# Performance work log

Measured on AMD Instinct MI355X. Metric: run time of the kernel, lower is better.

The kernel has to match this reference:

```python
import jax, jax.numpy as jnp
import numpy as np

N_HEADS = 28
N_KV_HEADS = 4
HEAD_DIM = 128
ROPE_THETA = 1000000.0


def _sinusoidal_positions(num_pos, dim, theta):
    # Mirrors create_sinusoidal_positions: interleaved [sin, cos] pairs -> (num_pos, dim)
    positions = jnp.arange(0, num_pos, dtype=jnp.float32)
    half_dim = dim // 2
    freq_indices = jnp.arange(0, half_dim, dtype=jnp.float32)
    inv_freq = 1.0 / theta ** (freq_indices / half_dim)
    sinusoid_inp = jnp.einsum('i,j->ij', positions, inv_freq)
    return jnp.stack([jnp.sin(sinusoid_inp), jnp.cos(sinusoid_inp)], axis=-1).reshape(num_pos, -1)


def _rotate_half(x):
    x1, x2 = jnp.split(x, 2, axis=-1)
    return jnp.concatenate([-x2, x1], axis=-1)


def _apply_rope(q, k, sinu_pos):
    # Mirrors apply_rotary_pos_emb: split halves, duplicate, rotate_half mixing.
    sin, cos = jnp.split(sinu_pos, 2, axis=-1)
    sin = jnp.concatenate([sin, sin], axis=-1)[None, None, :, :]
    cos = jnp.concatenate([cos, cos], axis=-1)[None, None, :, :]
    q_embed = q * cos + _rotate_half(q) * sin
    k_embed = k * cos + _rotate_half(k) * sin
    return q_embed, k_embed


def setup_inputs() -> dict:
    key = jax.random.key(0)
    ks = jax.random.split(key, 5)
    B, S, H = 2, 2048, 3584
    std = 0.02
    return {
        'hidden_states': jax.random.normal(ks[0], (B, S, H), dtype=jnp.float32),
        'wq': jax.random.normal(ks[1], (H, N_HEADS * HEAD_DIM), dtype=jnp.float32) * std,
        'wk': jax.random.normal(ks[2], (H, N_KV_HEADS * HEAD_DIM), dtype=jnp.float32) * std,
        'wv': jax.random.normal(ks[3], (H, N_KV_HEADS * HEAD_DIM), dtype=jnp.float32) * std,
        'wo': jax.random.normal(ks[4], (N_HEADS * HEAD_DIM, H), dtype=jnp.float32) * std,
    }


def reference(hidden_states, wq, wk, wv, wo):
    B, S, H = hidden_states.shape
    gqa_ratio = N_HEADS // N_KV_HEADS

    # QKV projections (bias-free) and head split -> (B, heads, S, d)
    q = (hidden_states @ wq).reshape(B, S, N_HEADS, HEAD_DIM).transpose(0, 2, 1, 3)
    k = (hidden_states @ wk).reshape(B, S, N_KV_HEADS, HEAD_DIM).transpose(0, 2, 1, 3)
    v = (hidden_states @ wv).reshape(B, S, N_KV_HEADS, HEAD_DIM).transpose(0, 2, 1, 3)

    # Inline RoPE on Q/K
    sincos = _sinusoidal_positions(S, HEAD_DIM, ROPE_THETA)
    q, k = _apply_rope(q, k, sincos)

    # GQA head expansion via tile (matches jnp.tile in source: block-repeat)
    k = jnp.tile(k, (1, gqa_ratio, 1, 1))
    v = jnp.tile(v, (1, gqa_ratio, 1, 1))

    # Causal scaled dot-product attention
    scale = 1.0 / jnp.sqrt(jnp.float32(HEAD_DIM))
    scores = jnp.einsum('bhqd,bhkd->bhqk', q, k) * scale  # (B, H, S, S)
    causal = jnp.tril(jnp.ones((S, S), dtype=bool))
    scores = jnp.where(causal[None, None], scores, jnp.finfo(scores.dtype).min)
    probs = jax.nn.softmax(scores, axis=-1)
    out = jnp.einsum('bhqk,bhkd->bhqd', probs, v)

    # Merge heads and output projection
    out = out.transpose(0, 2, 1, 3).reshape(B, S, N_HEADS * HEAD_DIM)
    return out @ wo
```

## Files before the change

kernel.cpp:

```cpp
#include <hip/hip_runtime.h>
#include <hip/hip_bf16.h>

typedef __attribute__((ext_vector_type(4))) float f32x4;
typedef __attribute__((ext_vector_type(8))) short s16x8;
typedef __attribute__((ext_vector_type(4))) short s16x4;
typedef unsigned short u16;

__device__ __forceinline__ u16 f2bf(float f) {
  union { float f; unsigned int u; } v; v.f = f;
  unsigned int r = v.u + 0x7fffu + ((v.u >> 16) & 1u);
  return (u16)(r >> 16);
}

__device__ __forceinline__ void gload_lds16(const void* g, void* l) {
  __builtin_amdgcn_global_load_lds(
      (const __attribute__((address_space(1))) void*)g,
      (__attribute__((address_space(3))) void*)l, 16, 0, 0);
}

__global__ __launch_bounds__(256) void cvt_bf16(const float* __restrict__ in,
                                                u16* __restrict__ outp, int nquad) {
  int i = blockIdx.x * 256 + threadIdx.x;
  if (i >= nquad) return;
  f32x4 v = *(const f32x4*)(in + (size_t)i * 4);
  s16x4 o;
  o.x = (short)f2bf(v.x); o.y = (short)f2bf(v.y);
  o.z = (short)f2bf(v.z); o.w = (short)f2bf(v.w);
  *(s16x4*)(outp + (size_t)i * 4) = o;
}

__global__ __launch_bounds__(256) void transpose_cvt(const float* __restrict__ in,
                                                     u16* __restrict__ outp, int R, int C) {
  __shared__ float t[32][33];
  int c0 = blockIdx.x * 32, r0 = blockIdx.y * 32;
  int tx = threadIdx.x & 31, ty = threadIdx.x >> 5;
#pragma unroll
  for (int i = 0; i < 32; i += 8) t[ty + i][tx] = in[(size_t)(r0 + ty + i) * C + c0 + tx];
  __syncthreads();
#pragma unroll
  for (int i = 0; i < 32; i += 8)
    outp[(size_t)(c0 + ty + i) * R + r0 + tx] = f2bf(t[tx][ty + i]);
}

__global__ void rope_table(float2* __restrict__ tab) {
  int p = blockIdx.x, e = threadIdx.x;
  int j = e >> 1;
  float f1 = powf(1.0e6f, -(float)j / 64.0f);
  float f2 = powf(1.0e6f, -(float)(j + 32) / 64.0f);
  float a1 = (float)p * f1, a2 = (float)p * f2;
  float S = (e & 1) ? cosf(a1) : sinf(a1);
  float C = (e & 1) ? cosf(a2) : sinf(a2);
  tab[p * 64 + e] = make_float2(S, C);
}

__global__ __launch_bounds__(256) void rope_pack(const float* __restrict__ P,
                                                 const float2* __restrict__ tab,
                                                 u16* __restrict__ outp, int nh, int ldp,
                                                 float scale) {
  int idx = blockIdx.x * 4 + (threadIdx.x >> 6);
  int e = threadIdx.x & 63;
  int s = idx & 2047;
  int bh = idx >> 11;
  int b = bh / nh, h = bh - b * nh;
  size_t prow = ((size_t)(b * 2048 + s)) * (size_t)ldp + (size_t)h * 128;
  float x1 = P[prow + e], x2 = P[prow + e + 64];
  float2 t = tab[s * 64 + e];
  float o1 = (x1 * t.y - x2 * t.x) * scale;
  float o2 = (x2 * t.y + x1 * t.x) * scale;
  size_t orow = (size_t)idx * 128;
  outp[orow + e] = f2bf(o1);
  outp[orow + e + 64] = f2bf(o2);
}

__global__ __launch_bounds__(256) void pack_vt(const float* __restrict__ Vp,
                                               u16* __restrict__ Vt, int ldp, int coff) {
  __shared__ float t[32][33];
  int bk = blockIdx.z;
  int b = bk >> 2, kh = bk & 3;
  int s0 = blockIdx.x * 32, d0 = blockIdx.y * 32;
  int tx = threadIdx.x & 31, ty = threadIdx.x >> 5;
  const float* in = Vp + (size_t)(b * 2048) * ldp + coff + kh * 128;
#pragma unroll
  for (int i = 0; i < 32; i += 8) t[ty + i][tx] = in[(size_t)(s0 + ty + i) * ldp + d0 + tx];
  __syncthreads();
  u16* outp = Vt + (size_t)bk * 128 * 2048;
#pragma unroll
  for (int i = 0; i < 32; i += 8)
    outp[(size_t)(d0 + ty + i) * 2048 + s0 + tx] = f2bf(t[tx][ty + i]);
}

__global__ __launch_bounds__(256) void gemm_bt(const u16* __restrict__ A,
                                               const u16* __restrict__ BT,
                                               float* __restrict__ C, int M, int N, int K) {
  __shared__ u16 lA[128 * 32];
  __shared__ u16 lB[128 * 32];
  const int tid = threadIdx.x;
  const int lane = tid & 63, wave = tid >> 6;
  const int bm = blockIdx.y * 128, bn = blockIdx.x * 128;
  const int wr = (wave >> 1) * 64, wc = (wave & 1) * 64;
  const int r = lane & 15, g = lane >> 4;

  f32x4 acc[4][4];
#pragma unroll
  for (int i = 0; i < 4; i++)
#pragma unroll
    for (int j = 0; j < 4; j++) acc[i][j] = (f32x4){0.f, 0.f, 0.f, 0.f};

  const int o0 = wave * 2048 + lane * 16;
  const int row0 = o0 >> 6, cb0 = (o0 & 63) >> 1;
  const int o1 = o0 + 1024;
  const int row1 = o1 >> 6, cb1 = (o1 & 63) >> 1;
  const u16* a0 = A + (size_t)(bm + row0) * K + cb0;
  const u16* a1 = A + (size_t)(bm + row1) * K + cb1;
  const u16* b0 = BT + (size_t)(bn + row0) * K + cb0;
  const u16* b1 = BT + (size_t)(bn + row1) * K + cb1;
  u16* lA0 = lA + wave * 2 * 512; u16* lA1 = lA + (wave * 2 + 1) * 512;
  u16* lB0 = lB + wave * 2 * 512; u16* lB1 = lB + (wave * 2 + 1) * 512;

  for (int kt = 0; kt < K; kt += 32) {
    __syncthreads();
    gload_lds16(a0 + kt, lA0);
    gload_lds16(a1 + kt, lA1);
    gload_lds16(b0 + kt, lB0);
    gload_lds16(b1 + kt, lB1);
    __syncthreads();
    s16x8 af[4], bf[4];
#pragma unroll
    for (int m2 = 0; m2 < 4; m2++) af[m2] = *(const s16x8*)(lA + (wr + m2 * 16 + r) * 32 + g * 8);
#pragma unroll
    for (int n2 = 0; n2 < 4; n2++) bf[n2] = *(const s16x8*)(lB + (wc + n2 * 16 + r) * 32 + g * 8);
#pragma unroll
    for (int m2 = 0; m2 < 4; m2++)
#pragma unroll
      for (int n2 = 0; n2 < 4; n2++)
        acc[m2][n2] = __builtin_amdgcn_mfma_f32_16x16x32_bf16(af[m2], bf[n2], acc[m2][n2], 0, 0, 0);
  }
#pragma unroll
  for (int m2 = 0; m2 < 4; m2++)
#pragma unroll
    for (int n2 = 0; n2 < 4; n2++)
#pragma unroll
      for (int jj = 0; jj < 4; jj++)
        C[(size_t)(bm + wr + m2 * 16 + g * 4 + jj) * N + (bn + wc + n2 * 16 + r)] =
            acc[m2][n2][jj];
}

__global__ __launch_bounds__(512, 2) void gemm256(const u16* __restrict__ A,
                                                  const u16* __restrict__ BT,
                                                  float* __restrict__ C,
                                                  int M, int N, int K) {
  extern __shared__ u16 sm[];
  const int tid = threadIdx.x;
  const int lane = tid & 63, w = tid >> 6;
  const int wm = w >> 2, wn = w & 3;
  const int r = lane & 15, g = lane >> 4;
  const int bm = blockIdx.y * 256, bn = blockIdx.x * 256;

  f32x4 acc[8][4];
#pragma unroll
  for (int mf = 0; mf < 8; mf++)
#pragma unroll
    for (int nf = 0; nf < 4; nf++) acc[mf][nf] = (f32x4){0.f, 0.f, 0.f, 0.f};

  const int row_s = tid >> 3;
  const int col_s = ((((tid & 7) << 4) ^ ((row_s & 7) << 4)) >> 1);
  const u16* sAg[4]; const u16* sBg[4];
#pragma unroll
  for (int i = 0; i < 4; i++) {
    sAg[i] = A  + (size_t)(bm + i * 64 + row_s) * K + col_s;
    sBg[i] = BT + (size_t)(bn + i * 64 + row_s) * K + col_s;
  }

#pragma unroll
  for (int i = 0; i < 4; i++) gload_lds16(sAg[i], sm + i * 4096 + w * 512);
#pragma unroll
  for (int i = 0; i < 4; i++) gload_lds16(sBg[i], sm + 32768 + i * 4096 + w * 512);

  const int NT = K >> 6;
  const int swz = (r & 7) << 4;
#pragma unroll 1
  for (int t = 0; t < NT; ++t) {
    const int p = t & 1;
    const u16* LA = sm + p * 16384;
    const u16* LB = sm + 32768 + p * 16384;
    u16* SA = sm + (p ^ 1) * 16384;
    u16* SB = sm + 32768 + (p ^ 1) * 16384;
    const int ktn = (t + 1 < NT) ? (t + 1) * 64 : 0;

    __builtin_amdgcn_s_barrier();
    gload_lds16(sAg[0] + ktn, SA + 0 * 4096 + w * 512);
    gload_lds16(sAg[1] + ktn, SA + 1 * 4096 + w * 512);
    asm volatile("s_waitcnt vmcnt(2)" ::: "memory");
    __builtin_amdgcn_s_barrier();
    __builtin_amdgcn_sched_barrier(0);

    const char* Ac = (const char*)LA;
    const char* Bc = (const char*)LB;
    s16x8 bf[4][2];
#pragma unroll
    for (int nf = 0; nf < 4; nf++)
#pragma unroll
      for (int ks = 0; ks < 2; ks++) {
        int row = wn * 64 + nf * 16 + r;
        bf[nf][ks] = *(const s16x8*)(Bc + ((row * 128 + ks * 64 + g * 16) ^ swz));
      }
#pragma unroll
    for (int ph = 0; ph < 4; ph++) {
      if (ph == 1) {
        gload_lds16(sAg[2] + ktn, SA + 2 * 4096 + w * 512);
        gload_lds16(sAg[3] + ktn, SA + 3 * 4096 + w * 512);
      } else if (ph == 2) {
        gload_lds16(sBg[0] + ktn, SB + 0 * 4096 + w * 512);
        gload_lds16(sBg[1] + ktn, SB + 1 * 4096 + w * 512);
      } else if (ph == 3) {
        gload_lds16(sBg[2] + ktn, SB + 2 * 4096 + w * 512);
        gload_lds16(sBg[3] + ktn, SB + 3 * 4096 + w * 512);
      }
      s16x8 af[2][2];
#pragma unroll
      for (int mi = 0; mi < 2; mi++)
#pragma unroll
        for (int ks = 0; ks < 2; ks++) {
          int row = wm * 128 + (ph * 2 + mi) * 16 + r;
          af[mi][ks] = *(const s16x8*)(Ac + ((row * 128 + ks * 64 + g * 16) ^ swz));
        }
      __builtin_amdgcn_s_setprio(1);
#pragma unroll
      for (int mi = 0; mi < 2; mi++)
#pragma unroll
        for (int nf = 0; nf < 4; nf++) {
          acc[ph * 2 + mi][nf] = __builtin_amdgcn_mfma_f32_16x16x32_bf16(
              af[mi][0], bf[nf][0], acc[ph * 2 + mi][nf], 0, 0, 0);
          acc[ph * 2 + mi][nf] = __builtin_amdgcn_mfma_f32_16x16x32_bf16(
              af[mi][1], bf[nf][1], acc[ph * 2 + mi][nf], 0, 0, 0);
        }
      __builtin_amdgcn_s_setprio(0);
    }
  }
  asm volatile("s_waitcnt vmcnt(0)" ::: "memory");

#pragma unroll
  for (int mf = 0; mf < 8; mf++)
#pragma unroll
    for (int nf = 0; nf < 4; nf++)
#pragma unroll
      for (int jj = 0; jj < 4; jj++)
        C[(size_t)(bm + wm * 128 + mf * 16 + g * 4 + jj) * N +
          (bn + wn * 64 + nf * 16 + r)] = acc[mf][nf][jj];
}

__global__ __launch_bounds__(512, 4) void attn_kernel(const u16* __restrict__ Q,
                                                      const u16* __restrict__ K,
                                                      const u16* __restrict__ Vt,
                                                      u16* __restrict__ AO) {
  constexpr int S = 2048, NH = 28, NKV = 4, D = 128;
  __shared__ u16 Kl[2][32 * 128];
  __shared__ u16 Vl[2][32 * 128];
  const int tid = threadIdx.x;
  const int lane = tid & 63, w = tid >> 6;
  const int r = lane & 15, g = lane >> 4;
  const int pp = blockIdx.x, h = blockIdx.y, b = blockIdx.z;
  const int kh = h & 3;
  const u16* Kb = K + ((size_t)(b * NKV + kh) * S) * D;
  const u16* Vb = Vt + ((size_t)(b * NKV + kh) * D) * S;

  const int o = tid * 16;
  const int krow = o >> 8;
  const int kcol = ((o & 255) ^ ((krow & 7) << 4)) >> 1;
  const u16* sK = Kb + (size_t)krow * D + kcol;
  const int pb = o ^ (((o >> 7) & 7) << 4);
  const u16* sV = Vb + (size_t)(pb >> 6) * S + ((pb & 63) >> 1);

#pragma unroll 1
  for (int seg = 0; seg < 2; ++seg) {
    const int qt = seg ? (15 - pp) : pp;
    const int q0 = qt * 128 + w * 16;
    const u16* Qb = Q + ((size_t)(b * NH + h) * S + q0) * D;

    s16x8 qf[4];
#pragma unroll
    for (int kb = 0; kb < 4; kb++)
      qf[kb] = *(const s16x8*)(Qb + (size_t)r * D + kb * 32 + g * 8);

    f32x4 o8[8];
#pragma unroll
    for (int c = 0; c < 8; c++) o8[c] = (f32x4){0.f, 0.f, 0.f, 0.f};
    float m = -1e30f, lsum = 0.f;
    const int qg = q0 + r;
    const int NT = 4 * qt + 4;

    gload_lds16(sK, (u16*)Kl[0] + tid * 8);
    gload_lds16(sV, (u16*)Vl[0] + tid * 8);

    int cur = 0;
#pragma unroll 1
    for (int t = 0; t < NT; ++t) {
      const int j = t * 32;
      if (t + 1 < NT) {
        const int jn = j + 32;
        gload_lds16(sK + (size_t)jn * D, (u16*)Kl[cur ^ 1] + tid * 8);
        gload_lds16(sV + jn, (u16*)Vl[cur ^ 1] + tid * 8);
        asm volatile("s_waitcnt vmcnt(2)" ::: "memory");
      } else {
        asm volatile("s_waitcnt vmcnt(0)" ::: "memory");
      }
      __builtin_amdgcn_s_barrier();
      __builtin_amdgcn_sched_barrier(0);
      if (j <= q0 + 15) {
        f32x4 st0 = (f32x4){0.f, 0.f, 0.f, 0.f};
        f32x4 st1 = (f32x4){0.f, 0.f, 0.f, 0.f};
        const int swz = (r & 7) << 4;
        const char* Kc = (const char*)Kl[cur];
        __builtin_amdgcn_s_setprio(1);
#pragma unroll
        for (int kb = 0; kb < 4; kb++) {
          int cb = (kb * 64 + g * 16) ^ swz;
          s16x8 kf = *(const s16x8*)(Kc + r * 256 + cb);
          st0 = __builtin_amdgcn_mfma_f32_16x16x32_bf16(kf, qf[kb], st0, 0, 0, 0);
        }
#pragma unroll
        for (int kb = 0; kb < 4; kb++) {
          int cb = (kb * 64 + g * 16) ^ swz;
          s16x8 kf = *(const s16x8*)(Kc + (r + 16) * 256 + cb);
          st1 = __builtin_amdgcn_mfma_f32_16x16x32_bf16(kf, qf[kb], st1, 0, 0, 0);
        }
        __builtin_amdgcn_s_setprio(0);
        float s8v[8];
        if (j + 31 <= q0) {
#pragma unroll
          for (int jj = 0; jj < 4; jj++) { s8v[jj] = st0[jj]; s8v[jj + 4] = st1[jj]; }
        } else {
#pragma unroll
          for (int jj = 0; jj < 4; jj++) {
            int kv0 = j + g * 4 + jj;
            s8v[jj] = (kv0 > qg) ? -1e30f : st0[jj];
            s8v[jj + 4] = (kv0 + 16 > qg) ? -1e30f : st1[jj];
          }
        }
        float pm = fmaxf(fmaxf(fmaxf(s8v[0], s8v[1]), fmaxf(s8v[2], s8v[3])),
                         fmaxf(fmaxf(s8v[4], s8v[5]), fmaxf(s8v[6], s8v[7])));
        pm = fmaxf(pm, __shfl_xor(pm, 16));
        pm = fmaxf(pm, __shfl_xor(pm, 32));
        const bool defer = __all(pm <= m + 8.f);
        float mnew, fr;
        if (defer) { mnew = m; fr = 1.f; }
        else { mnew = fmaxf(m, pm); fr = __expf(m - mnew); }
        float pv[8], psum = 0.f;
#pragma unroll
        for (int i2 = 0; i2 < 8; i2++) { pv[i2] = __expf(s8v[i2] - mnew); psum += pv[i2]; }
        psum += __shfl_xor(psum, 16);
        psum += __shfl_xor(psum, 32);
        lsum = lsum * fr + psum;
        m = mnew;
        unsigned pk[4];
#pragma unroll
        for (int i2 = 0; i2 < 4; i2++) {
          __hip_bfloat162 hv = __float22bfloat162_rn(make_float2(pv[2 * i2], pv[2 * i2 + 1]));
          union { __hip_bfloat162 h; unsigned u; } cv; cv.h = hv; pk[i2] = cv.u;
        }
        int L0 = r + ((g & 1) << 5);
        unsigned a0 = (unsigned)__shfl((int)pk[0], L0);
        unsigned a1 = (unsigned)__shfl((int)pk[1], L0);
        unsigned a2 = (unsigned)__shfl((int)pk[2], L0);
        unsigned a3 = (unsigned)__shfl((int)pk[3], L0);
        unsigned b0 = (unsigned)__shfl((int)pk[0], L0 + 16);
        unsigned b1 = (unsigned)__shfl((int)pk[1], L0 + 16);
        unsigned b2 = (unsigned)__shfl((int)pk[2], L0 + 16);
        unsigned b3 = (unsigned)__shfl((int)pk[3], L0 + 16);
        union { unsigned u[4]; s16x8 v; } pu;
        pu.u[0] = (g < 2) ? a0 : a2;
        pu.u[1] = (g < 2) ? a1 : a3;
        pu.u[2] = (g < 2) ? b0 : b2;
        pu.u[3] = (g < 2) ? b1 : b3;
        s16x8 pa = pu.v;
        float fB[4];
        if (!defer) {
#pragma unroll
          for (int jj = 0; jj < 4; jj++) fB[jj] = __shfl(fr, g * 4 + jj);
        }
        const char* Vc = (const char*)Vl[cur];
        __builtin_amdgcn_s_setprio(1);
#pragma unroll
        for (int c = 0; c < 8; c++) {
          int pbyte = (c * 16 + r) * 64 + g * 16;
          int vaddr = pbyte ^ ((r >> 1) << 4);
          s16x8 vf = *(const s16x8*)(Vc + vaddr);
          f32x4 oc = o8[c];
          if (!defer) { oc.x *= fB[0]; oc.y *= fB[1]; oc.z *= fB[2]; oc.w *= fB[3]; }
          o8[c] = __builtin_amdgcn_mfma_f32_16x16x32_bf16(pa, vf, oc, 0, 0, 0);
        }
        __builtin_amdgcn_s_setprio(0);
      }
      __builtin_amdgcn_s_barrier();
      cur ^= 1;
    }

    float lB[4];
#pragma unroll
    for (int jj = 0; jj < 4; jj++) lB[jj] = __shfl(lsum, g * 4 + jj);
#pragma unroll
    for (int c = 0; c < 8; c++)
#pragma unroll
      for (int jj = 0; jj < 4; jj++) {
        float val = o8[c][jj] / lB[jj];
        AO[(size_t)(b * S + q0 + g * 4 + jj) * 3584 + h * 128 + c * 16 + r] = f2bf(val);
      }
  }
}

static const size_t OFF_XBF = 0;
static const size_t OFF_WQT = 29360128;
static const size_t OFF_WKT = 55050240;
static const size_t OFF_WVT = 58720256;
static const size_t OFF_WOT = 62390272;
static const size_t OFF_TAB = 88080384;
static const size_t OFF_QBF = 89128960;
static const size_t OFF_KBF = 118489088;
static const size_t OFF_VT  = 122683392;
static const size_t OFF_QP  = 126877696;
static const size_t OFF_KVP = 185597952;

extern "C" void kernel_launch(void* const* d_in, const int* in_sizes, int n_in,
                              void* d_out, int out_size, void* d_ws, size_t ws_size,
                              hipStream_t stream) {
  const float* X  = (const float*)d_in[0];
  const float* Wq = (const float*)d_in[1];
  const float* Wk = (const float*)d_in[2];
  const float* Wv = (const float*)d_in[3];
  const float* Wo = (const float*)d_in[4];
  float* out = (float*)d_out;
  char* ws = (char*)d_ws;

  u16* Xbf = (u16*)(ws + OFF_XBF);
  u16* WqT = (u16*)(ws + OFF_WQT);
  u16* WkT = (u16*)(ws + OFF_WKT);
  u16* WvT = (u16*)(ws + OFF_WVT);
  u16* WoT = (u16*)(ws + OFF_WOT);
  float2* tab = (float2*)(ws + OFF_TAB);
  u16* Qbf = (u16*)(ws + OFF_QBF);
  u16* Kbf = (u16*)(ws + OFF_KBF);
  u16* Vtb = (u16*)(ws + OFF_VT);
  float* Qp = (float*)(ws + OFF_QP);
  float* KVp = (float*)(ws + OFF_KVP);
  u16* AO  = (u16*)(ws + OFF_QP);

  hipFuncSetAttribute((const void*)gemm256,
                      hipFuncAttributeMaxDynamicSharedMemorySize, 131072);

  cvt_bf16<<<14336, 256, 0, stream>>>(X, Xbf, 3670016);
  transpose_cvt<<<dim3(112, 112), 256, 0, stream>>>(Wq, WqT, 3584, 3584);
  transpose_cvt<<<dim3(16, 112), 256, 0, stream>>>(Wk, WkT, 3584, 512);
  transpose_cvt<<<dim3(16, 112), 256, 0, stream>>>(Wv, WvT, 3584, 512);
  transpose_cvt<<<dim3(112, 112), 256, 0, stream>>>(Wo, WoT, 3584, 3584);
  rope_table<<<2048, 64, 0, stream>>>(tab);

  gemm256<<<dim3(14, 16), 512, 131072, stream>>>(Xbf, WqT, Qp, 4096, 3584, 3584);
  gemm_bt<<<dim3(8, 32), 256, 0, stream>>>(Xbf, WkT, KVp, 4096, 1024, 3584);

  rope_pack<<<28672, 256, 0, stream>>>(Qp, tab, Qbf, 28, 3584, 0.08838834764831845f);
  rope_pack<<<4096, 256, 0, stream>>>(KVp, tab, Kbf, 4, 1024, 1.0f);
  pack_vt<<<dim3(64, 4, 8), 256, 0, stream>>>(KVp, Vtb, 1024, 512);

  attn_kernel<<<dim3(8, 28, 2), 512, 0, stream>>>(Qbf, Kbf, Vtb, AO);

  gemm256<<<dim3(14, 16), 512, 131072, stream>>>(AO, WoT, out, 4096, 3584, 3584);
}
```

Measured before the change: 513.4 us.

## Fuse QKV projection into one bf16-output GEMM and retile attention to 64-row blocks

Drops the separate K/V GEMM and runs one 256-tile GEMM over the concatenated Wq/Wk/Wv transposes, which sit contiguously in the workspace. That GEMM writes bf16 output, so rope_pack and pack_vt now read bf16 instead of fp32, halving intermediate traffic. The attention kernel moves from 512-thread blocks over 128 query rows to 256-thread blocks over 64 query rows with twice as many blocks. It also defers the cross-lane max and sum shuffles until they are needed. Rounding the projections to bf16 before RoPE adds a small precision loss.

```diff
diff --git a/kernel.cpp b/kernel.cpp
--- a/kernel.cpp
+++ b/kernel.cpp
@@ -10,6 +10,9 @@
   union { float f; unsigned int u; } v; v.f = f;
   unsigned int r = v.u + 0x7fffu + ((v.u >> 16) & 1u);
   return (u16)(r >> 16);
+}
+__device__ __forceinline__ float bf2f(u16 x) {
+  union { unsigned u; float f; } v; v.u = ((unsigned)x) << 16; return v.f;
 }
 
 __device__ __forceinline__ void gload_lds16(const void* g, void* l) {
@@ -53,17 +56,17 @@
   tab[p * 64 + e] = make_float2(S, C);
 }
 
-__global__ __launch_bounds__(256) void rope_pack(const float* __restrict__ P,
+__global__ __launch_bounds__(256) void rope_pack(const u16* __restrict__ P,
                                                  const float2* __restrict__ tab,
                                                  u16* __restrict__ outp, int nh, int ldp,
-                                                 float scale) {
+                                                 int coff, float scale) {
   int idx = blockIdx.x * 4 + (threadIdx.x >> 6);
   int e = threadIdx.x & 63;
   int s = idx & 2047;
   int bh = idx >> 11;
   int b = bh / nh, h = bh - b * nh;
-  size_t prow = ((size_t)(b * 2048 + s)) * (size_t)ldp + (size_t)h * 128;
-  float x1 = P[prow + e], x2 = P[prow + e + 64];
+  size_t prow = ((size_t)(b * 2048 + s)) * (size_t)ldp + coff + (size_t)h * 128;
+  float x1 = bf2f(P[prow + e]), x2 = bf2f(P[prow + e + 64]);
   float2 t = tab[s * 64 + e];
   float o1 = (x1 * t.y - x2 * t.x) * scale;
   float o2 = (x2 * t.y + x1 * t.x) * scale;
@@ -72,82 +75,27 @@
   outp[orow + e + 64] = f2bf(o2);
 }
 
-__global__ __launch_bounds__(256) void pack_vt(const float* __restrict__ Vp,
+__global__ __launch_bounds__(256) void pack_vt(const u16* __restrict__ P,
                                                u16* __restrict__ Vt, int ldp, int coff) {
-  __shared__ float t[32][33];
+  __shared__ u16 t[32][33];
   int bk = blockIdx.z;
   int b = bk >> 2, kh = bk & 3;
   int s0 = blockIdx.x * 32, d0 = blockIdx.y * 32;
   int tx = threadIdx.x & 31, ty = threadIdx.x >> 5;
-  const float* in = Vp + (size_t)(b * 2048) * ldp + coff + kh * 128;
+  const u16* in = P + (size_t)(b * 2048) * ldp + coff + kh * 128;
 #pragma unroll
   for (int i = 0; i < 32; i += 8) t[ty + i][tx] = in[(size_t)(s0 + ty + i) * ldp + d0 + tx];
   __syncthreads();
   u16* outp = Vt + (size_t)bk * 128 * 2048;
 #pragma unroll
   for (int i = 0; i < 32; i += 8)
-    outp[(size_t)(d0 + ty + i) * 2048 + s0 + tx] = f2bf(t[tx][ty + i]);
-}
-
-__global__ __launch_bounds__(256) void gemm_bt(const u16* __restrict__ A,
-                                               const u16* __restrict__ BT,
-                                               float* __restrict__ C, int M, int N, int K) {
-  __shared__ u16 lA[128 * 32];
-  __shared__ u16 lB[128 * 32];
-  const int tid = threadIdx.x;
-  const int lane = tid & 63, wave = tid >> 6;
-  const int bm = blockIdx.y * 128, bn = blockIdx.x * 128;
-  const int wr = (wave >> 1) * 64, wc = (wave & 1) * 64;
-  const int r = lane & 15, g = lane >> 4;
-
-  f32x4 acc[4][4];
-#pragma unroll
-  for (int i = 0; i < 4; i++)
-#pragma unroll
-    for (int j = 0; j < 4; j++) acc[i][j] = (f32x4){0.f, 0.f, 0.f, 0.f};
-
-  const int o0 = wave * 2048 + lane * 16;
-  const int row0 = o0 >> 6, cb0 = (o0 & 63) >> 1;
-  const int o1 = o0 + 1024;
-  const int row1 = o1 >> 6, cb1 = (o1 & 63) >> 1;
-  const u16* a0 = A + (size_t)(bm + row0) * K + cb0;
-  const u16* a1 = A + (size_t)(bm + row1) * K + cb1;
-  const u16* b0 = BT + (size_t)(bn + row0) * K + cb0;
-  const u16* b1 = BT + (size_t)(bn + row1) * K + cb1;
-  u16* lA0 = lA + wave * 2 * 512; u16* lA1 = lA + (wave * 2 + 1) * 512;
-  u16* lB0 = lB + wave * 2 * 512; u16* lB1 = lB + (wave * 2 + 1) * 512;
-
-  for (int kt = 0; kt < K; kt += 32) {
-    __syncthreads();
-    gload_lds16(a0 + kt, lA0);
-    gload_lds16(a1 + kt, lA1);
-    gload_lds16(b0 + kt, lB0);
-    gload_lds16(b1 + kt, lB1);
-    __syncthreads();
-    s16x8 af[4], bf[4];
-#pragma unroll
-    for (int m2 = 0; m2 < 4; m2++) af[m2] = *(const s16x8*)(lA + (wr + m2 * 16 + r) * 32 + g * 8);
-#pragma unroll
-    for (int n2 = 0; n2 < 4; n2++) bf[n2] = *(const s16x8*)(lB + (wc + n2 * 16 + r) * 32 + g * 8);
-#pragma unroll
-    for (int m2 = 0; m2 < 4; m2++)
-#pragma unroll
-      for (int n2 = 0; n2 < 4; n2++)
-        acc[m2][n2] = __builtin_amdgcn_mfma_f32_16x16x32_bf16(af[m2], bf[n2], acc[m2][n2], 0, 0, 0);
-  }
-#pragma unroll
-  for (int m2 = 0; m2 < 4; m2++)
-#pragma unroll
-    for (int n2 = 0; n2 < 4; n2++)
-#pragma unroll
-      for (int jj = 0; jj < 4; jj++)
-        C[(size_t)(bm + wr + m2 * 16 + g * 4 + jj) * N + (bn + wc + n2 * 16 + r)] =
-            acc[m2][n2][jj];
-}
-
+    outp[(size_t)(d0 + ty + i) * 2048 + s0 + tx] = t[tx][ty + i];
+}
+
+template <int OUT_BF16>
 __global__ __launch_bounds__(512, 2) void gemm256(const u16* __restrict__ A,
                                                   const u16* __restrict__ BT,
-                                                  float* __restrict__ C,
+                                                  void* __restrict__ Cv,
                                                   int M, int N, int K) {
   extern __shared__ u16 sm[];
   const int tid = threadIdx.x;
@@ -244,12 +192,15 @@
 #pragma unroll
     for (int nf = 0; nf < 4; nf++)
 #pragma unroll
-      for (int jj = 0; jj < 4; jj++)
-        C[(size_t)(bm + wm * 128 + mf * 16 + g * 4 + jj) * N +
-          (bn + wn * 64 + nf * 16 + r)] = acc[mf][nf][jj];
-}
-
-__global__ __launch_bounds__(512, 4) void attn_kernel(const u16* __restrict__ Q,
+      for (int jj = 0; jj < 4; jj++) {
+        size_t idx = (size_t)(bm + wm * 128 + mf * 16 + g * 4 + jj) * N +
+                     (bn + wn * 64 + nf * 16 + r);
+        if constexpr (OUT_BF16) ((u16*)Cv)[idx] = f2bf(acc[mf][nf][jj]);
+        else                    ((float*)Cv)[idx] = acc[mf][nf][jj];
+      }
+}
+
+__global__ __launch_bounds__(256, 4) void attn_kernel(const u16* __restrict__ Q,
                                                       const u16* __restrict__ K,
                                                       const u16* __restrict__ Vt,
                                                       u16* __restrict__ AO) {
@@ -264,17 +215,21 @@
   const u16* Kb = K + ((size_t)(b * NKV + kh) * S) * D;
   const u16* Vb = Vt + ((size_t)(b * NKV + kh) * D) * S;
 
-  const int o = tid * 16;
-  const int krow = o >> 8;
-  const int kcol = ((o & 255) ^ ((krow & 7) << 4)) >> 1;
-  const u16* sK = Kb + (size_t)krow * D + kcol;
-  const int pb = o ^ (((o >> 7) & 7) << 4);
-  const u16* sV = Vb + (size_t)(pb >> 6) * S + ((pb & 63) >> 1);
+  const u16 *sK[2], *sV[2];
+#pragma unroll
+  for (int i = 0; i < 2; i++) {
+    int o = i * 4096 + tid * 16;
+    int krow = o >> 8;
+    int kcol = ((o & 255) ^ ((krow & 7) << 4)) >> 1;
+    sK[i] = Kb + (size_t)krow * D + kcol;
+    int p = o ^ (((o >> 7) & 7) << 4);
+    sV[i] = Vb + (size_t)(p >> 6) * S + ((p & 63) >> 1);
+  }
 
 #pragma unroll 1
   for (int seg = 0; seg < 2; ++seg) {
-    const int qt = seg ? (15 - pp) : pp;
-    const int q0 = qt * 128 + w * 16;
+    const int qt = seg ? (31 - pp) : pp;
+    const int q0 = qt * 64 + w * 16;
     const u16* Qb = Q + ((size_t)(b * NH + h) * S + q0) * D;
 
     s16x8 qf[4];
@@ -287,20 +242,26 @@
     for (int c = 0; c < 8; c++) o8[c] = (f32x4){0.f, 0.f, 0.f, 0.f};
     float m = -1e30f, lsum = 0.f;
     const int qg = q0 + r;
-    const int NT = 4 * qt + 4;
-
-    gload_lds16(sK, (u16*)Kl[0] + tid * 8);
-    gload_lds16(sV, (u16*)Vl[0] + tid * 8);
+    const int NT = 2 * qt + 2;
+
+#pragma unroll
+    for (int i = 0; i < 2; i++) {
+      gload_lds16(sK[i], (u16*)Kl[0] + i * 2048 + tid * 8);
+      gload_lds16(sV[i], (u16*)Vl[0] + i * 2048 + tid * 8);
+    }
 
     int cur = 0;
 #pragma unroll 1
     for (int t = 0; t < NT; ++t) {
       const int j = t * 32;
       if (t + 1 < NT) {
-        const int jn = j + 32;
-        gload_lds16(sK + (size_t)jn * D, (u16*)Kl[cur ^ 1] + tid * 8);
-        gload_lds16(sV + jn, (u16*)Vl[cur ^ 1] + tid * 8);
-        asm volatile("s_waitcnt vmcnt(2)" ::: "memory");
+        const size_t jn = (size_t)(j + 32);
+#pragma unroll
+        for (int i = 0; i < 2; i++) {
+          gload_lds16(sK[i] + jn * D, (u16*)Kl[cur ^ 1] + i * 2048 + tid * 8);
+          gload_lds16(sV[i] + jn,     (u16*)Vl[cur ^ 1] + i * 2048 + tid * 8);
+        }
+        asm volatile("s_waitcnt vmcnt(4)" ::: "memory");
       } else {
         asm volatile("s_waitcnt vmcnt(0)" ::: "memory");
       }
@@ -339,19 +300,19 @@
         }
         float pm = fmaxf(fmaxf(fmaxf(s8v[0], s8v[1]), fmaxf(s8v[2], s8v[3])),
                          fmaxf(fmaxf(s8v[4], s8v[5]), fmaxf(s8v[6], s8v[7])));
-        pm = fmaxf(pm, __shfl_xor(pm, 16));
-        pm = fmaxf(pm, __shfl_xor(pm, 32));
         const bool defer = __all(pm <= m + 8.f);
-        float mnew, fr;
-        if (defer) { mnew = m; fr = 1.f; }
-        else { mnew = fmaxf(m, pm); fr = __expf(m - mnew); }
+        float fr = 1.f;
+        if (!defer) {
+          pm = fmaxf(pm, __shfl_xor(pm, 16));
+          pm = fmaxf(pm, __shfl_xor(pm, 32));
+          float mnew = fmaxf(m, pm);
+          fr = __expf(m - mnew);
+          m = mnew;
+        }
         float pv[8], psum = 0.f;
 #pragma unroll
-        for (int i2 = 0; i2 < 8; i2++) { pv[i2] = __expf(s8v[i2] - mnew); psum += pv[i2]; }
-        psum += __shfl_xor(psum, 16);
-        psum += __shfl_xor(psum, 32);
+        for (int i2 = 0; i2 < 8; i2++) { pv[i2] = __expf(s8v[i2] - m); psum += pv[i2]; }
         lsum = lsum * fr + psum;
-        m = mnew;
         unsigned pk[4];
 #pragma unroll
         for (int i2 = 0; i2 < 4; i2++) {
@@ -395,9 +356,12 @@
       cur ^= 1;
     }
 
+    float lrow = lsum;
+    lrow += __shfl_xor(lrow, 16);
+    lrow += __shfl_xor(lrow, 32);
     float lB[4];
 #pragma unroll
-    for (int jj = 0; jj < 4; jj++) lB[jj] = __shfl(lsum, g * 4 + jj);
+    for (int jj = 0; jj < 4; jj++) lB[jj] = __shfl(lrow, g * 4 + jj);
 #pragma unroll
     for (int c = 0; c < 8; c++)
 #pragma unroll
@@ -417,8 +381,8 @@
 static const size_t OFF_QBF = 89128960;
 static const size_t OFF_KBF = 118489088;
 static const size_t OFF_VT  = 122683392;
-static const size_t OFF_QP  = 126877696;
-static const size_t OFF_KVP = 185597952;
+static const size_t OFF_QKV = 126877696;
+static const size_t OFF_AO  = 164626432;
 
 extern "C" void kernel_launch(void* const* d_in, const int* in_sizes, int n_in,
                               void* d_out, int out_size, void* d_ws, size_t ws_size,
@@ -440,11 +404,12 @@
   u16* Qbf = (u16*)(ws + OFF_QBF);
   u16* Kbf = (u16*)(ws + OFF_KBF);
   u16* Vtb = (u16*)(ws + OFF_VT);
-  float* Qp = (float*)(ws + OFF_QP);
-  float* KVp = (float*)(ws + OFF_KVP);
-  u16* AO  = (u16*)(ws + OFF_QP);
-
-  hipFuncSetAttribute((const void*)gemm256,
+  u16* QKV = (u16*)(ws + OFF_QKV);
+  u16* AO  = (u16*)(ws + OFF_AO);
+
+  hipFuncSetAttribute(reinterpret_cast<const void*>(gemm256<1>),
+                      hipFuncAttributeMaxDynamicSharedMemorySize, 131072);
+  hipFuncSetAttribute(reinterpret_cast<const void*>(gemm256<0>),
                       hipFuncAttributeMaxDynamicSharedMemorySize, 131072);
 
   cvt_bf16<<<14336, 256, 0, stream>>>(X, Xbf, 3670016);
@@ -454,14 +419,13 @@
   transpose_cvt<<<dim3(112, 112), 256, 0, stream>>>(Wo, WoT, 3584, 3584);
   rope_table<<<2048, 64, 0, stream>>>(tab);
 
-  gemm256<<<dim3(14, 16), 512, 131072, stream>>>(Xbf, WqT, Qp, 4096, 3584, 3584);
-  gemm_bt<<<dim3(8, 32), 256, 0, stream>>>(Xbf, WkT, KVp, 4096, 1024, 3584);
-
-  rope_pack<<<28672, 256, 0, stream>>>(Qp, tab, Qbf, 28, 3584, 0.08838834764831845f);
-  rope_pack<<<4096, 256, 0, stream>>>(KVp, tab, Kbf, 4, 1024, 1.0f);
-  pack_vt<<<dim3(64, 4, 8), 256, 0, stream>>>(KVp, Vtb, 1024, 512);
-
-  attn_kernel<<<dim3(8, 28, 2), 512, 0, stream>>>(Qbf, Kbf, Vtb, AO);
-
-  gemm256<<<dim3(14, 16), 512, 131072, stream>>>(AO, WoT, out, 4096, 3584, 3584);
-}
+  gemm256<1><<<dim3(18, 16), 512, 131072, stream>>>(Xbf, WqT, QKV, 4096, 4608, 3584);
+
+  rope_pack<<<28672, 256, 0, stream>>>(QKV, tab, Qbf, 28, 4608, 0, 0.08838834764831845f);
+  rope_pack<<<4096, 256, 0, stream>>>(QKV, tab, Kbf, 4, 4608, 3584, 1.0f);
+  pack_vt<<<dim3(64, 4, 8), 256, 0, stream>>>(QKV, Vtb, 4608, 4096);
+
+  attn_kernel<<<dim3(16, 28, 2), 256, 0, stream>>>(Qbf, Kbf, Vtb, AO);
+
+  gemm256<0><<<dim3(14, 16), 512, 131072, stream>>>(AO, WoT, out, 4096, 3584, 3584);
+}
```

After: 510.2 us (median of 2 runs). About the same (-0.6%).
